# Performance work log

Measured on AMD Instinct MI355X. Metric: run time of the kernel, lower is better.

The kernel has to match this reference:

```python
import jax, jax.numpy as jnp
import numpy as np
from jax import lax

NUM_BLOCKS = 3
NUM_LAYERS = 10
NL = NUM_BLOCKS * NUM_LAYERS  # 30 res blocks
RC = 512   # residual channels
GC = 512   # gate channels
SC = 512   # skip channels
KS = 2     # kernel size
CIN = 128  # local-conditioning channels
FRONT = 32 # front conv kernel size
OUT = 2    # gaussian (mean, log_std)
UPS = [16, 16]  # upsample scales, product = 256 hop
SQRT_HALF = 0.7071067811865476


def causal_conv1d(x, w, b, dilation):
    # x: [B,C_in,T], w: [C_out,C_in,K] -> left-pad only == torch pad-both + trim right (causal SAME)
    pad = dilation * (w.shape[-1] - 1)
    y = lax.conv_general_dilated(x, w, window_strides=(1,), padding=[(pad, 0)],
                                 rhs_dilation=(dilation,),
                                 dimension_numbers=('NCH', 'OIH', 'NCH'))
    return y + b[None, :, None]


def pw(x, w, b):
    # 1x1 conv: w [C_out,C_in]
    return jnp.einsum('oi,bit->bot', w, x) + b[None, :, None]


def upsample(c, up_w, up_b):
    # c: [B,CIN,Tm]; torch ConvTranspose2d(1,1,(3,2s),pad=(1,s//2),stride=(1,s)) + LeakyReLU(0.4)
    h = c[:, None]  # [B,1,CIN,Tm]
    for j, s in enumerate(UPS):
        k = up_w[j][:, :, ::-1, ::-1]  # flip kernel: transposed conv as lhs-dilated conv
        pw_ = 2 * s - 1 - s // 2       # = K - 1 - torch_pad along width
        h = lax.conv_general_dilated(h, k, window_strides=(1, 1),
                                     padding=[(1, 1), (pw_, pw_)],
                                     lhs_dilation=(1, s),
                                     dimension_numbers=('NCHW', 'OIHW', 'NCHW')) + up_b[j]
        h = jnp.where(h > 0, h, 0.4 * h)  # LeakyReLU(0.4)
    return h[:, 0]  # [B,CIN,T]


def setup_inputs() -> dict:
    key = jax.random.key(0)
    ks = iter(jax.random.split(key, 32))
    def rn(shape, scale):
        return jax.random.normal(next(ks), shape, dtype=jnp.float32) * scale
    B, T_mel = 1, 16
    T = T_mel * 256
    return {
        'x': rn((B, 1, T), 1.0),
        'c': rn((B, CIN, T_mel), 1.0),
        'front_w': rn((RC, 1, FRONT), 0.2),
        'front_b': rn((RC,), 0.05),
        'filt_w': rn((NL, GC, RC, KS), 0.03),
        'filt_b': rn((NL, GC), 0.05),
        'gate_w': rn((NL, GC, RC, KS), 0.03),
        'gate_b': rn((NL, GC), 0.05),
        'cf_w': rn((NL, GC, CIN), 0.05),
        'cf_b': rn((NL, GC), 0.05),
        'cg_w': rn((NL, GC, CIN), 0.05),
        'cg_b': rn((NL, GC), 0.05),
        'res_w': rn((NL, RC, GC), 0.04),
        'res_b': rn((NL, RC), 0.05),
        'skip_w': rn((NL, SC, GC), 0.04),
        'skip_b': rn((NL, SC), 0.05),
        'fin1_w': rn((SC, SC), 0.04),
        'fin1_b': rn((SC,), 0.05),
        'fin2_w': rn((OUT, SC), 0.04),
        'fin2_b': rn((OUT,), 0.05),
        'up_w': rn((2, 1, 1, 3, 2 * 16), 0.1),
        'up_b': rn((2,), 0.05),
    }


def reference(x, c, front_w, front_b, filt_w, filt_b, gate_w, gate_b,
              cf_w, cf_b, cg_w, cg_b, res_w, res_b, skip_w, skip_b,
              fin1_w, fin1_b, fin2_w, fin2_b, up_w, up_b):
    c_up = upsample(c, up_w, up_b)                       # [B,CIN,T]
    h = jax.nn.relu(causal_conv1d(x, front_w, front_b, 1))  # [B,RC,T]
    skip = jnp.zeros((x.shape[0], SC, x.shape[2]), x.dtype)
    for i in range(NL):
        d = KS ** (i % NUM_LAYERS)
        f = causal_conv1d(h, filt_w[i], filt_b[i], d) + pw(c_up, cf_w[i], cf_b[i])
        g = causal_conv1d(h, gate_w[i], gate_b[i], d) + pw(c_up, cg_w[i], cg_b[i])
        o = jnp.tanh(f) * jax.nn.sigmoid(g)
        h = (h + pw(o, res_w[i], res_b[i])) * SQRT_HALF
        skip = skip + pw(o, skip_w[i], skip_b[i])
    out = jax.nn.relu(skip)
    out = jax.nn.relu(pw(out, fin1_w, fin1_b))
    return pw(out, fin2_w, fin2_b)  # [B,OUT,T]
```

## Files before the change

kernel.cpp:

```cpp
#include <hip/hip_runtime.h>
#include <hip/hip_bf16.h>

#define TLEN 4096
#define HPADT 512
#define SQRT_HALF 0.70710678118654752f

typedef __attribute__((ext_vector_type(8))) short short8;
typedef __attribute__((ext_vector_type(4))) float floatx4;
typedef __attribute__((ext_vector_type(4))) unsigned short ushort4v;

#define MFMA_BF16(a, b, c) __builtin_amdgcn_mfma_f32_16x16x32_bf16((a), (b), (c), 0, 0, 0)

__device__ __forceinline__ float bf2f(unsigned short u) {
  union { unsigned int i; float f; } v; v.i = ((unsigned int)u) << 16; return v.f;
}
__device__ __forceinline__ unsigned short f2bf(float x) {
  union { float f; unsigned int i; } v; v.f = x;
  unsigned int r = v.i + 0x7FFFu + ((v.i >> 16) & 1u);
  return (unsigned short)(r >> 16);
}
__device__ __forceinline__ short8 ld8(const unsigned short* p) { return *(const short8*)p; }

template <int NI>
__device__ __forceinline__ void stage128(unsigned short* lds, const unsigned short* src,
                                         int stride, int tid) {
  #pragma unroll
  for (int inst = 0; inst < NI; ++inst) {
    int qb = inst * 256 + (tid & 192);
    int q = qb + (tid & 63);
    int r = q >> 4;
    int c = (q & 15) ^ (r & 15);
    __builtin_amdgcn_global_load_lds(
        (const __attribute__((address_space(1))) unsigned int*)(src + (size_t)r * stride + (c << 3)),
        (__attribute__((address_space(3))) unsigned int*)(lds + qb * 8),
        16, 0, 0);
  }
}
__device__ __forceinline__ short8 frag128(const unsigned short* lds, int r, int cj) {
  return *(const short8*)(lds + r * 128 + ((cj ^ (r & 15)) << 3));
}

template <int NI>
__device__ __forceinline__ void stage64(unsigned short* lds, const unsigned short* src,
                                        int stride, int tid) {
  #pragma unroll
  for (int inst = 0; inst < NI; ++inst) {
    int qb = inst * 256 + (tid & 192);
    int q = qb + (tid & 63);
    int r = q >> 3;
    int c = (q & 7) ^ (r & 7);
    __builtin_amdgcn_global_load_lds(
        (const __attribute__((address_space(1))) unsigned int*)(src + (size_t)r * stride + (c << 3)),
        (__attribute__((address_space(3))) unsigned int*)(lds + qb * 8),
        16, 0, 0);
  }
}
__device__ __forceinline__ short8 frag64(const unsigned short* lds, int r, int cj) {
  return *(const short8*)(lds + r * 64 + ((cj ^ (r & 7)) << 3));
}

__device__ __forceinline__ void wait_vm12() { asm volatile("s_waitcnt vmcnt(12)" ::: "memory"); }
__device__ __forceinline__ void wait_vm6()  { asm volatile("s_waitcnt vmcnt(6)"  ::: "memory"); }
__device__ __forceinline__ void wait_vm0()  { asm volatile("s_waitcnt vmcnt(0)"  ::: "memory"); }

__global__ __launch_bounds__(256) void cast_all_kernel(
    const float* __restrict__ fw, const float* __restrict__ gw,
    const float* __restrict__ rw, const float* __restrict__ sw,
    const float* __restrict__ cf, const float* __restrict__ cg,
    const float* __restrict__ f1, const float* __restrict__ fb,
    const float* __restrict__ cfb, const float* __restrict__ gb,
    const float* __restrict__ cgb,
    unsigned short* __restrict__ WA, unsigned short* __restrict__ RS,
    unsigned short* __restrict__ CA, unsigned short* __restrict__ F1c,
    float* __restrict__ fgb)
{
  int b = blockIdx.x;
  if (b < 7680) {
    size_t idx = (size_t)b * 256 + threadIdx.x;
    size_t l = idx >> 16;
    int o = (int)((idx >> 7) & 511);
    int i4 = (int)(idx & 127) * 4;
    const float4* fp = (const float4*)(fw + (((l * 512 + o) * 512 + i4) * 2));
    const float4* gp = (const float4*)(gw + (((l * 512 + o) * 512 + i4) * 2));
    float4 f0 = fp[0], f1v = fp[1];
    float4 g0 = gp[0], g1 = gp[1];
    size_t base0 = ((l * 2 + 0) * 1024);
    size_t base1 = ((l * 2 + 1) * 1024);
    *(ushort4v*)&WA[(base0 + o) * 512 + i4]       = (ushort4v){f2bf(f0.x), f2bf(f0.z), f2bf(f1v.x), f2bf(f1v.z)};
    *(ushort4v*)&WA[(base1 + o) * 512 + i4]       = (ushort4v){f2bf(f0.y), f2bf(f0.w), f2bf(f1v.y), f2bf(f1v.w)};
    *(ushort4v*)&WA[(base0 + 512 + o) * 512 + i4] = (ushort4v){f2bf(g0.x), f2bf(g0.z), f2bf(g1.x), f2bf(g1.z)};
    *(ushort4v*)&WA[(base1 + 512 + o) * 512 + i4] = (ushort4v){f2bf(g0.y), f2bf(g0.w), f2bf(g1.y), f2bf(g1.w)};
  } else if (b < 15360) {
    size_t idx = (size_t)(b - 7680) * 256 + threadIdx.x;
    size_t l = idx >> 16;
    int o = (int)((idx >> 7) & 511);
    int i4 = (int)(idx & 127) * 4;
    float4 r4 = *(const float4*)(rw + ((l * 512 + o) * 512 + i4));
    float4 s4 = *(const float4*)(sw + ((l * 512 + o) * 512 + i4));
    *(ushort4v*)&RS[(l * 1024 + o) * 512 + i4]       = (ushort4v){f2bf(r4.x), f2bf(r4.y), f2bf(r4.z), f2bf(r4.w)};
    *(ushort4v*)&RS[(l * 1024 + 512 + o) * 512 + i4] = (ushort4v){f2bf(s4.x), f2bf(s4.y), f2bf(s4.z), f2bf(s4.w)};
  } else if (b < 17280) {
    size_t idx = (size_t)(b - 15360) * 256 + threadIdx.x;
    size_t l = idx >> 14;
    int o = (int)((idx >> 5) & 511);
    int i4 = (int)(idx & 31) * 4;
    float4 f4 = *(const float4*)(cf + ((l * 512 + o) * 128 + i4));
    float4 g4 = *(const float4*)(cg + ((l * 512 + o) * 128 + i4));
    *(ushort4v*)&CA[(l * 1024 + o) * 128 + i4]       = (ushort4v){f2bf(f4.x), f2bf(f4.y), f2bf(f4.z), f2bf(f4.w)};
    *(ushort4v*)&CA[(l * 1024 + 512 + o) * 128 + i4] = (ushort4v){f2bf(g4.x), f2bf(g4.y), f2bf(g4.z), f2bf(g4.w)};
  } else if (b < 17536) {
    size_t idx = (size_t)(b - 17280) * 256 + threadIdx.x;
    float4 v = *(const float4*)(f1 + idx * 4);
    *(ushort4v*)&F1c[idx * 4] = (ushort4v){f2bf(v.x), f2bf(v.y), f2bf(v.z), f2bf(v.w)};
  } else {
    int idx = (b - 17536) * 256 + threadIdx.x;
    int l = idx >> 10, r = idx & 1023;
    float v;
    if (r < 512) v = fb[l * 512 + r] + cfb[l * 512 + r];
    else         v = gb[l * 512 + r - 512] + cgb[l * 512 + r - 512];
    fgb[idx] = v;
  }
}


__global__ __launch_bounds__(256) void upsample1_kernel(
    const float* __restrict__ c, const float* __restrict__ up_w,
    const float* __restrict__ up_b, float* __restrict__ u1)
{
  int x = threadIdx.x;
  int h = blockIdx.x;
  const float* w = up_w;
  float acc = 0.f;
  int k1 = (23 - x) & 15;
  #pragma unroll
  for (int dk = 0; dk < 2; ++dk) {
    int kx = k1 + 16 * dk;
    int num = x + kx - 23;
    if (num >= 0) {
      int qq = num >> 4;
      if (qq < 16) {
        #pragma unroll
        for (int ky = 0; ky < 3; ++ky) {
          int hh = h + ky - 1;
          if (hh >= 0 && hh < 128)
            acc += c[hh * 16 + qq] * w[(2 - ky) * 32 + (31 - kx)];
        }
      }
    }
  }
  acc += up_b[0];
  u1[h * 256 + x] = acc > 0.f ? acc : 0.4f * acc;
}

__global__ __launch_bounds__(256) void upsample2_kernel(
    const float* __restrict__ u1, const float* __restrict__ up_w,
    const float* __restrict__ up_b, unsigned short* __restrict__ cu)
{
  int x = blockIdx.x * 256 + threadIdx.x;
  int h = blockIdx.y;
  const float* w = up_w + 96;
  float acc = 0.f;
  int k1 = (23 - x) & 15;
  #pragma unroll
  for (int dk = 0; dk < 2; ++dk) {
    int kx = k1 + 16 * dk;
    int num = x + kx - 23;
    if (num >= 0) {
      int qq = num >> 4;
      if (qq < 256) {
        #pragma unroll
        for (int ky = 0; ky < 3; ++ky) {
          int hh = h + ky - 1;
          if (hh >= 0 && hh < 128)
            acc += u1[hh * 256 + qq] * w[(2 - ky) * 32 + (31 - kx)];
        }
      }
    }
  }
  acc += up_b[1];
  acc = acc > 0.f ? acc : 0.4f * acc;
  cu[(size_t)x * 128 + h] = f2bf(acc);
}

__global__ __launch_bounds__(256) void front_kernel(
    const float* __restrict__ x, const float* __restrict__ fw, const float* __restrict__ fb,
    float* __restrict__ hf, unsigned short* __restrict__ hbf)
{
  __shared__ float xs[40];
  int tid = threadIdx.x;
  int o = blockIdx.y * 256 + tid;
  int t0 = blockIdx.x * 8;
  if (tid < 39) {
    int gx = t0 - 31 + tid;
    xs[tid] = (gx >= 0) ? x[gx] : 0.f;
  }
  __syncthreads();
  float w[32];
  #pragma unroll
  for (int k = 0; k < 32; ++k) w[k] = fw[o * 32 + k];
  float b = fb[o];
  #pragma unroll
  for (int j = 0; j < 8; ++j) {
    float acc = b;
    #pragma unroll
    for (int k = 0; k < 32; ++k) acc += w[k] * xs[j + k];
    acc = acc > 0.f ? acc : 0.f;
    int t = t0 + j;
    hf[(size_t)t * 512 + o] = acc;
    hbf[(size_t)(HPADT + t) * 512 + o] = f2bf(acc);
  }
}

__global__ __launch_bounds__(256, 2) void gemm_a_kernel(
    const unsigned short* __restrict__ WA,
    const unsigned short* __restrict__ CA,
    const float* __restrict__ fgb,
    const unsigned short* __restrict__ hbf,
    const unsigned short* __restrict__ cu,
    unsigned short* __restrict__ obf,
    const int d)
{
  __shared__ unsigned short Af[3][32 * 64];
  __shared__ unsigned short Ag[3][32 * 64];
  __shared__ unsigned short Xs[3][128 * 64];

  const int tid = threadIdx.x;
  const int lane = tid & 63;
  const int wave = tid >> 6;
  const int lm = lane & 15, qd = lane >> 4;
  const int n0 = blockIdx.x * 128;
  const int m0 = blockIdx.y * 32;
  const int wn = wave * 32;
  const int NS = 18;

  floatx4 accF[2][2], accG[2][2];
  #pragma unroll
  for (int a = 0; a < 2; ++a)
    #pragma unroll
    for (int b = 0; b < 2; ++b) {
      accF[a][b] = (floatx4){0.f, 0.f, 0.f, 0.f};
      accG[a][b] = (floatx4){0.f, 0.f, 0.f, 0.f};
    }

  auto stage_step = [&](int s, int b) {
    if (s < 16) {
      int tap = s >> 3;
      int k0 = (s & 7) * 64;
      const unsigned short* ab = WA + (size_t)tap * 524288;
      stage64<1>(&Af[b][0], ab + (size_t)m0 * 512 + k0, 512, tid);
      stage64<1>(&Ag[b][0], ab + (size_t)(512 + m0) * 512 + k0, 512, tid);
      stage64<4>(&Xs[b][0], hbf + (size_t)(HPADT + n0 - (tap ? 0 : d)) * 512 + k0, 512, tid);
    } else {
      int k0 = (s - 16) * 64;
      stage64<1>(&Af[b][0], CA + (size_t)m0 * 128 + k0, 128, tid);
      stage64<1>(&Ag[b][0], CA + (size_t)(512 + m0) * 128 + k0, 128, tid);
      stage64<4>(&Xs[b][0], cu + (size_t)n0 * 128 + k0, 128, tid);
    }
  };

  stage_step(0, 0);
  stage_step(1, 1);
  int cur = 0;
  #pragma unroll 1
  for (int s = 0; s < NS; ++s) {
    int stg = cur + 2; if (stg >= 3) stg -= 3;
    if (s + 2 < NS) stage_step(s + 2, stg);
    if (s + 2 < NS)      wait_vm12();
    else if (s + 1 < NS) wait_vm6();
    else                 wait_vm0();
    __builtin_amdgcn_s_barrier();
    __builtin_amdgcn_sched_barrier(0);
    const unsigned short* af = &Af[cur][0];
    const unsigned short* ag = &Ag[cur][0];
    const unsigned short* xs = &Xs[cur][0];
    __builtin_amdgcn_s_setprio(1);
    #pragma unroll
    for (int j = 0; j < 2; ++j) {
      int cj = j * 4 + qd;
      short8 a0 = frag64(af, lm, cj);
      short8 a1 = frag64(af, 16 + lm, cj);
      short8 g0 = frag64(ag, lm, cj);
      short8 g1 = frag64(ag, 16 + lm, cj);
      short8 x0 = frag64(xs, wn + lm, cj);
      short8 x1 = frag64(xs, wn + 16 + lm, cj);
      accF[0][0] = MFMA_BF16(a0, x0, accF[0][0]);
      accF[0][1] = MFMA_BF16(a0, x1, accF[0][1]);
      accF[1][0] = MFMA_BF16(a1, x0, accF[1][0]);
      accF[1][1] = MFMA_BF16(a1, x1, accF[1][1]);
      accG[0][0] = MFMA_BF16(g0, x0, accG[0][0]);
      accG[0][1] = MFMA_BF16(g0, x1, accG[0][1]);
      accG[1][0] = MFMA_BF16(g1, x0, accG[1][0]);
      accG[1][1] = MFMA_BF16(g1, x1, accG[1][1]);
    }
    __builtin_amdgcn_s_setprio(0);
    __builtin_amdgcn_sched_barrier(0);
    __builtin_amdgcn_s_barrier();
    __builtin_amdgcn_sched_barrier(0);
    cur = (cur == 2) ? 0 : cur + 1;
  }

  #pragma unroll
  for (int mt = 0; mt < 2; ++mt) {
    int oc0 = m0 + mt * 16 + qd * 4;
    floatx4 fb4 = *(const floatx4*)&fgb[oc0];
    floatx4 gb4 = *(const floatx4*)&fgb[512 + oc0];
    #pragma unroll
    for (int nt = 0; nt < 2; ++nt) {
      int t = n0 + wn + nt * 16 + lm;
      ushort4v o4;
      #pragma unroll
      for (int r = 0; r < 4; ++r) {
        float f = accF[mt][nt][r] + fb4[r];
        float g = accG[mt][nt][r] + gb4[r];
        float ef = __expf(-2.f * f);
        float th = (1.f - ef) / (1.f + ef);
        float sg = 1.f / (1.f + __expf(-g));
        o4[r] = f2bf(th * sg);
      }
      *(ushort4v*)&obf[(size_t)t * 512 + oc0] = o4;
    }
  }
}

__global__ __launch_bounds__(256, 2) void gemm_b_kernel(
    const unsigned short* __restrict__ RS,
    const float* __restrict__ rb, const float* __restrict__ sb,
    const unsigned short* __restrict__ obf,
    float* __restrict__ hf, unsigned short* __restrict__ hbf,
    float* __restrict__ skip, unsigned short* __restrict__ skipbf,
    const int first, const int last)
{
  __shared__ unsigned short Ar[3][32 * 64];
  __shared__ unsigned short As_[3][32 * 64];
  __shared__ unsigned short Xs[3][128 * 64];

  const int tid = threadIdx.x;
  const int lane = tid & 63;
  const int wave = tid >> 6;
  const int lm = lane & 15, qd = lane >> 4;
  const int n0 = blockIdx.x * 128;
  const int m0 = blockIdx.y * 32;
  const int wn = wave * 32;
  const int NS = 8;

  floatx4 accR[2][2], accS[2][2];
  #pragma unroll
  for (int a = 0; a < 2; ++a)
    #pragma unroll
    for (int b = 0; b < 2; ++b) {
      accR[a][b] = (floatx4){0.f, 0.f, 0.f, 0.f};
      accS[a][b] = (floatx4){0.f, 0.f, 0.f, 0.f};
    }

  auto stage_step = [&](int s, int b) {
    int k0 = s * 64;
    stage64<1>(&Ar[b][0], RS + (size_t)m0 * 512 + k0, 512, tid);
    stage64<1>(&As_[b][0], RS + (size_t)(512 + m0) * 512 + k0, 512, tid);
    stage64<4>(&Xs[b][0], obf + (size_t)n0 * 512 + k0, 512, tid);
  };

  stage_step(0, 0);
  stage_step(1, 1);
  int cur = 0;
  #pragma unroll 1
  for (int s = 0; s < NS; ++s) {
    int stg = cur + 2; if (stg >= 3) stg -= 3;
    if (s + 2 < NS) stage_step(s + 2, stg);
    if (s + 2 < NS)      wait_vm12();
    else if (s + 1 < NS) wait_vm6();
    else                 wait_vm0();
    __builtin_amdgcn_s_barrier();
    __builtin_amdgcn_sched_barrier(0);
    const unsigned short* ar = &Ar[cur][0];
    const unsigned short* as = &As_[cur][0];
    const unsigned short* xs = &Xs[cur][0];
    __builtin_amdgcn_s_setprio(1);
    #pragma unroll
    for (int j = 0; j < 2; ++j) {
      int cj = j * 4 + qd;
      short8 a0 = frag64(ar, lm, cj);
      short8 a1 = frag64(ar, 16 + lm, cj);
      short8 g0 = frag64(as, lm, cj);
      short8 g1 = frag64(as, 16 + lm, cj);
      short8 x0 = frag64(xs, wn + lm, cj);
      short8 x1 = frag64(xs, wn + 16 + lm, cj);
      accR[0][0] = MFMA_BF16(a0, x0, accR[0][0]);
      accR[0][1] = MFMA_BF16(a0, x1, accR[0][1]);
      accR[1][0] = MFMA_BF16(a1, x0, accR[1][0]);
      accR[1][1] = MFMA_BF16(a1, x1, accR[1][1]);
      accS[0][0] = MFMA_BF16(g0, x0, accS[0][0]);
      accS[0][1] = MFMA_BF16(g0, x1, accS[0][1]);
      accS[1][0] = MFMA_BF16(g1, x0, accS[1][0]);
      accS[1][1] = MFMA_BF16(g1, x1, accS[1][1]);
    }
    __builtin_amdgcn_s_setprio(0);
    __builtin_amdgcn_sched_barrier(0);
    __builtin_amdgcn_s_barrier();
    __builtin_amdgcn_sched_barrier(0);
    cur = (cur == 2) ? 0 : cur + 1;
  }

  #pragma unroll
  for (int mt = 0; mt < 2; ++mt) {
    int oc0 = m0 + mt * 16 + qd * 4;
    floatx4 rb4 = *(const floatx4*)&rb[oc0];
    floatx4 sb4 = *(const floatx4*)&sb[oc0];
    #pragma unroll
    for (int nt = 0; nt < 2; ++nt) {
      int t = n0 + wn + nt * 16 + lm;
      size_t base = (size_t)t * 512 + oc0;
      floatx4 h4 = *(const floatx4*)&hf[base];
      floatx4 s4;
      if (first) s4 = (floatx4){0.f, 0.f, 0.f, 0.f};
      else s4 = *(const floatx4*)&skip[base];
      ushort4v hb4;
      #pragma unroll
      for (int r = 0; r < 4; ++r) {
        float hv = (h4[r] + accR[mt][nt][r] + rb4[r]) * SQRT_HALF;
        h4[r] = hv;
        hb4[r] = f2bf(hv);
        s4[r] = s4[r] + accS[mt][nt][r] + sb4[r];
      }
      *(floatx4*)&hf[base] = h4;
      *(ushort4v*)&hbf[(size_t)(HPADT + t) * 512 + oc0] = hb4;
      *(floatx4*)&skip[base] = s4;
      if (last) {
        ushort4v sk4;
        #pragma unroll
        for (int r = 0; r < 4; ++r) sk4[r] = f2bf(s4[r] > 0.f ? s4[r] : 0.f);
        *(ushort4v*)&skipbf[base] = sk4;
      }
    }
  }
}

__global__ __launch_bounds__(256) void final1_kernel(
    const unsigned short* __restrict__ W1,
    const float* __restrict__ b1,
    const unsigned short* __restrict__ skipbf,
    unsigned short* __restrict__ t1)
{
  __shared__ unsigned short Aw[2][64 * 128];
  __shared__ unsigned short Xs[2][128 * 128];

  const int tid = threadIdx.x;
  const int lane = tid & 63;
  const int wave = tid >> 6;
  const int lm = lane & 15, qd = lane >> 4;
  const int n0 = blockIdx.x * 128;
  const int m0 = blockIdx.y * 64;
  const int wm = (wave & 1) * 32;
  const int wn = (wave >> 1) * 64;

  floatx4 acc[2][4];
  #pragma unroll
  for (int a = 0; a < 2; ++a)
    #pragma unroll
    for (int b = 0; b < 4; ++b) acc[a][b] = (floatx4){0.f, 0.f, 0.f, 0.f};

  auto stage_step = [&](int s, int b) {
    int k0 = s * 128;
    stage128<4>(&Aw[b][0], W1 + (size_t)m0 * 512 + k0, 512, tid);
    stage128<8>(&Xs[b][0], skipbf + (size_t)n0 * 512 + k0, 512, tid);
  };

  stage_step(0, 0);
  for (int s = 0; s < 4; ++s) {
    __syncthreads();
    if (s < 3) stage_step(s + 1, (s + 1) & 1);
    const unsigned short* aw = &Aw[s & 1][0];
    const unsigned short* xs = &Xs[s & 1][0];
    #pragma unroll
    for (int j = 0; j < 4; ++j) {
      int cj = j * 4 + qd;
      short8 a[2], xv[4];
      a[0] = frag128(aw, wm + lm, cj);
      a[1] = frag128(aw, wm + 16 + lm, cj);
      #pragma unroll
      for (int nt = 0; nt < 4; ++nt) xv[nt] = frag128(xs, wn + nt * 16 + lm, cj);
      #pragma unroll
      for (int mt = 0; mt < 2; ++mt)
        #pragma unroll
        for (int nt = 0; nt < 4; ++nt)
          acc[mt][nt] = MFMA_BF16(a[mt], xv[nt], acc[mt][nt]);
    }
  }

  #pragma unroll
  for (int mt = 0; mt < 2; ++mt) {
    int oc0 = m0 + wm + mt * 16 + qd * 4;
    floatx4 b4 = *(const floatx4*)&b1[oc0];
    #pragma unroll
    for (int nt = 0; nt < 4; ++nt) {
      int t = n0 + wn + nt * 16 + lm;
      ushort4v o4;
      #pragma unroll
      for (int r = 0; r < 4; ++r) {
        float v = acc[mt][nt][r] + b4[r];
        o4[r] = f2bf(v > 0.f ? v : 0.f);
      }
      *(ushort4v*)&t1[(size_t)t * 512 + oc0] = o4;
    }
  }
}

__global__ __launch_bounds__(256) void final2_kernel(
    const float* __restrict__ W2, const float* __restrict__ b2,
    const unsigned short* __restrict__ t1, float* __restrict__ out)
{
  int wave = threadIdx.x >> 6, lane = threadIdx.x & 63;
  int t = blockIdx.x * 4 + wave;
  short8 v = ld8(t1 + (size_t)t * 512 + lane * 8);
  float a0 = 0.f, a1 = 0.f;
  #pragma unroll
  for (int r = 0; r < 8; ++r) {
    float f = bf2f((unsigned short)v[r]);
    a0 += W2[lane * 8 + r] * f;
    a1 += W2[512 + lane * 8 + r] * f;
  }
  #pragma unroll
  for (int off = 32; off > 0; off >>= 1) {
    a0 += __shfl_xor(a0, off, 64);
    a1 += __shfl_xor(a1, off, 64);
  }
  if (lane == 0) {
    out[t] = a0 + b2[0];
    out[TLEN + t] = a1 + b2[1];
  }
}

extern "C" void kernel_launch(void* const* d_in, const int* in_sizes, int n_in,
                              void* d_out, int out_size, void* d_ws, size_t ws_size,
                              hipStream_t stream) {
  (void)in_sizes; (void)n_in; (void)out_size; (void)ws_size;
  const float* x       = (const float*)d_in[0];
  const float* c       = (const float*)d_in[1];
  const float* front_w = (const float*)d_in[2];
  const float* front_b = (const float*)d_in[3];
  const float* filt_w  = (const float*)d_in[4];
  const float* filt_b  = (const float*)d_in[5];
  const float* gate_w  = (const float*)d_in[6];
  const float* gate_b  = (const float*)d_in[7];
  const float* cf_w    = (const float*)d_in[8];
  const float* cf_b    = (const float*)d_in[9];
  const float* cg_w    = (const float*)d_in[10];
  const float* cg_b    = (const float*)d_in[11];
  const float* res_w   = (const float*)d_in[12];
  const float* res_b   = (const float*)d_in[13];
  const float* skip_w  = (const float*)d_in[14];
  const float* skip_b  = (const float*)d_in[15];
  const float* fin1_w  = (const float*)d_in[16];
  const float* fin1_b  = (const float*)d_in[17];
  const float* fin2_w  = (const float*)d_in[18];
  const float* fin2_b  = (const float*)d_in[19];
  const float* up_w    = (const float*)d_in[20];
  const float* up_b    = (const float*)d_in[21];

  char* ws = (char*)d_ws;
  auto alloc = [&](size_t bytes) {
    char* p = ws;
    ws += (bytes + 255) & ~(size_t)255;
    return p;
  };
  unsigned short* WA     = (unsigned short*)alloc((size_t)30 * 2 * 1024 * 512 * 2);
  unsigned short* RS     = (unsigned short*)alloc((size_t)30 * 1024 * 512 * 2);
  unsigned short* CA     = (unsigned short*)alloc((size_t)30 * 1024 * 128 * 2);
  unsigned short* F1c    = (unsigned short*)alloc((size_t)512 * 512 * 2);
  float* fgb             = (float*)alloc((size_t)30 * 1024 * 4);
  float* u1              = (float*)alloc((size_t)128 * 256 * 4);
  unsigned short* cu     = (unsigned short*)alloc((size_t)TLEN * 128 * 2);
  float* hf              = (float*)alloc((size_t)TLEN * 512 * 4);
  unsigned short* hbf    = (unsigned short*)alloc((size_t)(HPADT + TLEN) * 512 * 2);
  unsigned short* obf    = (unsigned short*)alloc((size_t)TLEN * 512 * 2);
  float* skip            = (float*)alloc((size_t)TLEN * 512 * 4);
  unsigned short* skipbf = (unsigned short*)alloc((size_t)TLEN * 512 * 2);
  unsigned short* t1     = (unsigned short*)alloc((size_t)TLEN * 512 * 2);
  float* out             = (float*)d_out;

  hipMemsetAsync(hbf, 0, (size_t)HPADT * 512 * 2, stream);

  cast_all_kernel<<<17656, 256, 0, stream>>>(
      filt_w, gate_w, res_w, skip_w, cf_w, cg_w, fin1_w,
      filt_b, cf_b, gate_b, cg_b, WA, RS, CA, F1c, fgb);

  upsample1_kernel<<<dim3(128), 256, 0, stream>>>(c, up_w, up_b, u1);
  upsample2_kernel<<<dim3(16, 128), 256, 0, stream>>>(u1, up_w, up_b, cu);
  front_kernel<<<dim3(512, 2), 256, 0, stream>>>(x, front_w, front_b, hf, hbf);

  for (int l = 0; l < 30; ++l) {
    int d = 1 << (l % 10);
    gemm_a_kernel<<<dim3(32, 16), 256, 0, stream>>>(
        WA + (size_t)l * 2 * 524288, CA + (size_t)l * 131072,
        fgb + (size_t)l * 1024,
        hbf, cu, obf, d);
    gemm_b_kernel<<<dim3(32, 16), 256, 0, stream>>>(
        RS + (size_t)l * 524288,
        res_b + (size_t)l * 512, skip_b + (size_t)l * 512,
        obf, hf, hbf, skip, skipbf, (l == 0) ? 1 : 0, (l == 29) ? 1 : 0);
  }

  final1_kernel<<<dim3(32, 8), 256, 0, stream>>>(F1c, fin1_b, skipbf, t1);
  final2_kernel<<<1024, 256, 0, stream>>>(fin2_w, fin2_b, t1, out);
}
```

Baseline: 1.351 ms.

## Add small-dilation gate GEMM that reuses one staged time window for both taps

Adds a gemm_a variant for dilations up to 64 that stages a single contiguous window of h rows (tile width plus dilation) and reads both conv taps from it, instead of staging the two shifted input tiles separately. This is meant to cut global loads and LDS traffic for most layers. The h buffer gets extra tail padding so the over-wide window stays in bounds. The single weight-cast kernel is also split into several grid-stride launches, which adds launch overhead but changes the occupancy pattern of the cast.

```diff
diff --git a/kernel.cpp b/kernel.cpp
--- a/kernel.cpp
+++ b/kernel.cpp
@@ -63,20 +63,12 @@
 __device__ __forceinline__ void wait_vm6()  { asm volatile("s_waitcnt vmcnt(6)"  ::: "memory"); }
 __device__ __forceinline__ void wait_vm0()  { asm volatile("s_waitcnt vmcnt(0)"  ::: "memory"); }
 
-__global__ __launch_bounds__(256) void cast_all_kernel(
+__global__ __launch_bounds__(256) void cast_wa_kernel(
     const float* __restrict__ fw, const float* __restrict__ gw,
-    const float* __restrict__ rw, const float* __restrict__ sw,
-    const float* __restrict__ cf, const float* __restrict__ cg,
-    const float* __restrict__ f1, const float* __restrict__ fb,
-    const float* __restrict__ cfb, const float* __restrict__ gb,
-    const float* __restrict__ cgb,
-    unsigned short* __restrict__ WA, unsigned short* __restrict__ RS,
-    unsigned short* __restrict__ CA, unsigned short* __restrict__ F1c,
-    float* __restrict__ fgb)
-{
-  int b = blockIdx.x;
-  if (b < 7680) {
-    size_t idx = (size_t)b * 256 + threadIdx.x;
+    unsigned short* __restrict__ WA, int base, int count)
+{
+  for (int i = blockIdx.x * 256 + threadIdx.x; i < count; i += gridDim.x * 256) {
+    size_t idx = (size_t)base + i;
     size_t l = idx >> 16;
     int o = (int)((idx >> 7) & 511);
     int i4 = (int)(idx & 127) * 4;
@@ -90,8 +82,15 @@
     *(ushort4v*)&WA[(base1 + o) * 512 + i4]       = (ushort4v){f2bf(f0.y), f2bf(f0.w), f2bf(f1v.y), f2bf(f1v.w)};
     *(ushort4v*)&WA[(base0 + 512 + o) * 512 + i4] = (ushort4v){f2bf(g0.x), f2bf(g0.z), f2bf(g1.x), f2bf(g1.z)};
     *(ushort4v*)&WA[(base1 + 512 + o) * 512 + i4] = (ushort4v){f2bf(g0.y), f2bf(g0.w), f2bf(g1.y), f2bf(g1.w)};
-  } else if (b < 15360) {
-    size_t idx = (size_t)(b - 7680) * 256 + threadIdx.x;
+  }
+}
+
+__global__ __launch_bounds__(256) void cast_rs_kernel(
+    const float* __restrict__ rw, const float* __restrict__ sw,
+    unsigned short* __restrict__ RS, int base, int count)
+{
+  for (int i = blockIdx.x * 256 + threadIdx.x; i < count; i += gridDim.x * 256) {
+    size_t idx = (size_t)base + i;
     size_t l = idx >> 16;
     int o = (int)((idx >> 7) & 511);
     int i4 = (int)(idx & 127) * 4;
@@ -99,26 +98,40 @@
     float4 s4 = *(const float4*)(sw + ((l * 512 + o) * 512 + i4));
     *(ushort4v*)&RS[(l * 1024 + o) * 512 + i4]       = (ushort4v){f2bf(r4.x), f2bf(r4.y), f2bf(r4.z), f2bf(r4.w)};
     *(ushort4v*)&RS[(l * 1024 + 512 + o) * 512 + i4] = (ushort4v){f2bf(s4.x), f2bf(s4.y), f2bf(s4.z), f2bf(s4.w)};
-  } else if (b < 17280) {
-    size_t idx = (size_t)(b - 15360) * 256 + threadIdx.x;
-    size_t l = idx >> 14;
-    int o = (int)((idx >> 5) & 511);
-    int i4 = (int)(idx & 31) * 4;
-    float4 f4 = *(const float4*)(cf + ((l * 512 + o) * 128 + i4));
-    float4 g4 = *(const float4*)(cg + ((l * 512 + o) * 128 + i4));
-    *(ushort4v*)&CA[(l * 1024 + o) * 128 + i4]       = (ushort4v){f2bf(f4.x), f2bf(f4.y), f2bf(f4.z), f2bf(f4.w)};
-    *(ushort4v*)&CA[(l * 1024 + 512 + o) * 128 + i4] = (ushort4v){f2bf(g4.x), f2bf(g4.y), f2bf(g4.z), f2bf(g4.w)};
-  } else if (b < 17536) {
-    size_t idx = (size_t)(b - 17280) * 256 + threadIdx.x;
-    float4 v = *(const float4*)(f1 + idx * 4);
-    *(ushort4v*)&F1c[idx * 4] = (ushort4v){f2bf(v.x), f2bf(v.y), f2bf(v.z), f2bf(v.w)};
-  } else {
-    int idx = (b - 17536) * 256 + threadIdx.x;
-    int l = idx >> 10, r = idx & 1023;
-    float v;
-    if (r < 512) v = fb[l * 512 + r] + cfb[l * 512 + r];
-    else         v = gb[l * 512 + r - 512] + cgb[l * 512 + r - 512];
-    fgb[idx] = v;
+  }
+}
+
+__global__ __launch_bounds__(256) void cast_misc_kernel(
+    const float* __restrict__ cf, const float* __restrict__ cg,
+    const float* __restrict__ f1, const float* __restrict__ fb,
+    const float* __restrict__ cfb, const float* __restrict__ gb,
+    const float* __restrict__ cgb,
+    unsigned short* __restrict__ CA, unsigned short* __restrict__ F1c,
+    float* __restrict__ fgb)
+{
+  const int total = 491520 + 65536 + 30720;
+  for (int i = blockIdx.x * 256 + threadIdx.x; i < total; i += gridDim.x * 256) {
+    if (i < 491520) {
+      size_t idx = i;
+      size_t l = idx >> 14;
+      int o = (int)((idx >> 5) & 511);
+      int i4 = (int)(idx & 31) * 4;
+      float4 f4 = *(const float4*)(cf + ((l * 512 + o) * 128 + i4));
+      float4 g4 = *(const float4*)(cg + ((l * 512 + o) * 128 + i4));
+      *(ushort4v*)&CA[(l * 1024 + o) * 128 + i4]       = (ushort4v){f2bf(f4.x), f2bf(f4.y), f2bf(f4.z), f2bf(f4.w)};
+      *(ushort4v*)&CA[(l * 1024 + 512 + o) * 128 + i4] = (ushort4v){f2bf(g4.x), f2bf(g4.y), f2bf(g4.z), f2bf(g4.w)};
+    } else if (i < 491520 + 65536) {
+      size_t idx = i - 491520;
+      float4 v = *(const float4*)(f1 + idx * 4);
+      *(ushort4v*)&F1c[idx * 4] = (ushort4v){f2bf(v.x), f2bf(v.y), f2bf(v.z), f2bf(v.w)};
+    } else {
+      int idx = i - (491520 + 65536);
+      int l = idx >> 10, r = idx & 1023;
+      float v;
+      if (r < 512) v = fb[l * 512 + r] + cfb[l * 512 + r];
+      else         v = gb[l * 512 + r - 512] + cgb[l * 512 + r - 512];
+      fgb[idx] = v;
+    }
   }
 }
 
@@ -208,6 +221,135 @@
     int t = t0 + j;
     hf[(size_t)t * 512 + o] = acc;
     hbf[(size_t)(HPADT + t) * 512 + o] = f2bf(acc);
+  }
+}
+
+template <int XU>
+__global__ __launch_bounds__(256, 2) void gemm_a_smalld_kernel(
+    const unsigned short* __restrict__ WA,
+    const unsigned short* __restrict__ CA,
+    const float* __restrict__ fgb,
+    const unsigned short* __restrict__ hbf,
+    const unsigned short* __restrict__ cu,
+    unsigned short* __restrict__ obf,
+    const int d)
+{
+  __shared__ unsigned short U[2][XU * 32 * 64];
+  __shared__ unsigned short Aw[2][4][32 * 64];
+
+  const int tid = threadIdx.x;
+  const int lane = tid & 63;
+  const int wave = tid >> 6;
+  const int lm = lane & 15, qd = lane >> 4;
+  const int n0 = blockIdx.x * 128;
+  const int m0 = blockIdx.y * 32;
+  const int wn = wave * 32;
+  const int NS = 10;
+
+  floatx4 accF[2][2], accG[2][2];
+  #pragma unroll
+  for (int a = 0; a < 2; ++a)
+    #pragma unroll
+    for (int b = 0; b < 2; ++b) {
+      accF[a][b] = (floatx4){0.f, 0.f, 0.f, 0.f};
+      accG[a][b] = (floatx4){0.f, 0.f, 0.f, 0.f};
+    }
+
+  auto stage_step = [&](int s, int b) {
+    if (s < 8) {
+      int k0 = s * 64;
+      stage64<XU>(&U[b][0], hbf + (size_t)(HPADT + n0 - d) * 512 + k0, 512, tid);
+      stage64<1>(&Aw[b][0][0], WA + (size_t)m0 * 512 + k0, 512, tid);
+      stage64<1>(&Aw[b][1][0], WA + 524288 + (size_t)m0 * 512 + k0, 512, tid);
+      stage64<1>(&Aw[b][2][0], WA + (size_t)(512 + m0) * 512 + k0, 512, tid);
+      stage64<1>(&Aw[b][3][0], WA + 524288 + (size_t)(512 + m0) * 512 + k0, 512, tid);
+    } else {
+      int k0 = (s - 8) * 64;
+      stage64<4>(&U[b][0], cu + (size_t)n0 * 128 + k0, 128, tid);
+      stage64<1>(&Aw[b][0][0], CA + (size_t)m0 * 128 + k0, 128, tid);
+      stage64<1>(&Aw[b][2][0], CA + (size_t)(512 + m0) * 128 + k0, 128, tid);
+    }
+  };
+
+  stage_step(0, 0);
+  #pragma unroll 1
+  for (int s = 0; s < NS; ++s) {
+    __syncthreads();
+    if (s + 1 < NS) stage_step(s + 1, (s + 1) & 1);
+    const unsigned short* u   = &U[s & 1][0];
+    const unsigned short* af0 = &Aw[s & 1][0][0];
+    const unsigned short* af1 = &Aw[s & 1][1][0];
+    const unsigned short* ag0 = &Aw[s & 1][2][0];
+    const unsigned short* ag1 = &Aw[s & 1][3][0];
+    if (s < 8) {
+      #pragma unroll
+      for (int j = 0; j < 2; ++j) {
+        int cj = j * 4 + qd;
+        short8 f0a = frag64(af0, lm, cj),      f0b = frag64(af0, 16 + lm, cj);
+        short8 f1a = frag64(af1, lm, cj),      f1b = frag64(af1, 16 + lm, cj);
+        short8 g0a = frag64(ag0, lm, cj),      g0b = frag64(ag0, 16 + lm, cj);
+        short8 g1a = frag64(ag1, lm, cj),      g1b = frag64(ag1, 16 + lm, cj);
+        short8 x0 = frag64(u, wn + lm, cj);
+        short8 x1 = frag64(u, wn + 16 + lm, cj);
+        short8 y0 = frag64(u, d + wn + lm, cj);
+        short8 y1 = frag64(u, d + wn + 16 + lm, cj);
+        accF[0][0] = MFMA_BF16(f0a, x0, accF[0][0]);
+        accF[0][0] = MFMA_BF16(f1a, y0, accF[0][0]);
+        accF[0][1] = MFMA_BF16(f0a, x1, accF[0][1]);
+        accF[0][1] = MFMA_BF16(f1a, y1, accF[0][1]);
+        accF[1][0] = MFMA_BF16(f0b, x0, accF[1][0]);
+        accF[1][0] = MFMA_BF16(f1b, y0, accF[1][0]);
+        accF[1][1] = MFMA_BF16(f0b, x1, accF[1][1]);
+        accF[1][1] = MFMA_BF16(f1b, y1, accF[1][1]);
+        accG[0][0] = MFMA_BF16(g0a, x0, accG[0][0]);
+        accG[0][0] = MFMA_BF16(g1a, y0, accG[0][0]);
+        accG[0][1] = MFMA_BF16(g0a, x1, accG[0][1]);
+        accG[0][1] = MFMA_BF16(g1a, y1, accG[0][1]);
+        accG[1][0] = MFMA_BF16(g0b, x0, accG[1][0]);
+        accG[1][0] = MFMA_BF16(g1b, y0, accG[1][0]);
+        accG[1][1] = MFMA_BF16(g0b, x1, accG[1][1]);
+        accG[1][1] = MFMA_BF16(g1b, y1, accG[1][1]);
+      }
+    } else {
+      #pragma unroll
+      for (int j = 0; j < 2; ++j) {
+        int cj = j * 4 + qd;
+        short8 fa = frag64(af0, lm, cj), fbv = frag64(af0, 16 + lm, cj);
+        short8 ga = frag64(ag0, lm, cj), gbv = frag64(ag0, 16 + lm, cj);
+        short8 x0 = frag64(u, wn + lm, cj);
+        short8 x1 = frag64(u, wn + 16 + lm, cj);
+        accF[0][0] = MFMA_BF16(fa, x0, accF[0][0]);
+        accF[0][1] = MFMA_BF16(fa, x1, accF[0][1]);
+        accF[1][0] = MFMA_BF16(fbv, x0, accF[1][0]);
+        accF[1][1] = MFMA_BF16(fbv, x1, accF[1][1]);
+        accG[0][0] = MFMA_BF16(ga, x0, accG[0][0]);
+        accG[0][1] = MFMA_BF16(ga, x1, accG[0][1]);
+        accG[1][0] = MFMA_BF16(gbv, x0, accG[1][0]);
+        accG[1][1] = MFMA_BF16(gbv, x1, accG[1][1]);
+      }
+    }
+  }
+
+  #pragma unroll
+  for (int mt = 0; mt < 2; ++mt) {
+    int oc0 = m0 + mt * 16 + qd * 4;
+    floatx4 fb4 = *(const floatx4*)&fgb[oc0];
+    floatx4 gb4 = *(const floatx4*)&fgb[512 + oc0];
+    #pragma unroll
+    for (int nt = 0; nt < 2; ++nt) {
+      int t = n0 + wn + nt * 16 + lm;
+      ushort4v o4;
+      #pragma unroll
+      for (int r = 0; r < 4; ++r) {
+        float f = accF[mt][nt][r] + fb4[r];
+        float g = accG[mt][nt][r] + gb4[r];
+        float ef = __expf(-2.f * f);
+        float th = (1.f - ef) / (1.f + ef);
+        float sg = 1.f / (1.f + __expf(-g));
+        o4[r] = f2bf(th * sg);
+      }
+      *(ushort4v*)&obf[(size_t)t * 512 + oc0] = o4;
+    }
   }
 }
 
@@ -570,7 +712,7 @@
   float* u1              = (float*)alloc((size_t)128 * 256 * 4);
   unsigned short* cu     = (unsigned short*)alloc((size_t)TLEN * 128 * 2);
   float* hf              = (float*)alloc((size_t)TLEN * 512 * 4);
-  unsigned short* hbf    = (unsigned short*)alloc((size_t)(HPADT + TLEN) * 512 * 2);
+  unsigned short* hbf    = (unsigned short*)alloc((size_t)(HPADT + TLEN + 256) * 512 * 2);
   unsigned short* obf    = (unsigned short*)alloc((size_t)TLEN * 512 * 2);
   float* skip            = (float*)alloc((size_t)TLEN * 512 * 4);
   unsigned short* skipbf = (unsigned short*)alloc((size_t)TLEN * 512 * 2);
@@ -579,9 +721,12 @@
 
   hipMemsetAsync(hbf, 0, (size_t)HPADT * 512 * 2, stream);
 
-  cast_all_kernel<<<17656, 256, 0, stream>>>(
-      filt_w, gate_w, res_w, skip_w, cf_w, cg_w, fin1_w,
-      filt_b, cf_b, gate_b, cg_b, WA, RS, CA, F1c, fgb);
+  for (int g = 0; g < 6; ++g)
+    cast_wa_kernel<<<512, 256, 0, stream>>>(filt_w, gate_w, WA, g * 327680, 327680);
+  for (int g = 0; g < 6; ++g)
+    cast_rs_kernel<<<512, 256, 0, stream>>>(res_w, skip_w, RS, g * 327680, 327680);
+  cast_misc_kernel<<<512, 256, 0, stream>>>(cf_w, cg_w, fin1_w, filt_b, cf_b,
+                                            gate_b, cg_b, CA, F1c, fgb);
 
   upsample1_kernel<<<dim3(128), 256, 0, stream>>>(c, up_w, up_b, u1);
   upsample2_kernel<<<dim3(16, 128), 256, 0, stream>>>(u1, up_w, up_b, cu);
@@ -589,10 +734,19 @@
 
   for (int l = 0; l < 30; ++l) {
     int d = 1 << (l % 10);
-    gemm_a_kernel<<<dim3(32, 16), 256, 0, stream>>>(
-        WA + (size_t)l * 2 * 524288, CA + (size_t)l * 131072,
-        fgb + (size_t)l * 1024,
-        hbf, cu, obf, d);
+    if (d <= 32) {
+      gemm_a_smalld_kernel<5><<<dim3(32, 16), 256, 0, stream>>>(
+          WA + (size_t)l * 2 * 524288, CA + (size_t)l * 131072,
+          fgb + (size_t)l * 1024, hbf, cu, obf, d);
+    } else if (d == 64) {
+      gemm_a_smalld_kernel<6><<<dim3(32, 16), 256, 0, stream>>>(
+          WA + (size_t)l * 2 * 524288, CA + (size_t)l * 131072,
+          fgb + (size_t)l * 1024, hbf, cu, obf, d);
+    } else {
+      gemm_a_kernel<<<dim3(32, 16), 256, 0, stream>>>(
+          WA + (size_t)l * 2 * 524288, CA + (size_t)l * 131072,
+          fgb + (size_t)l * 1024, hbf, cu, obf, d);
+    }
     gemm_b_kernel<<<dim3(32, 16), 256, 0, stream>>>(
         RS + (size_t)l * 524288,
         res_b + (size_t)l * 512, skip_b + (size_t)l * 512,
```

New measurement: 1.281 ms. -5.2%, faster.
